# Performance work log

Measured on AMD Instinct MI355X. Metric: run time of the kernel, lower is better.

The kernel has to match this reference:

```python
import jax, jax.numpy as jnp
import numpy as np

NUM_HEADS = 16
NUM_GROUPS = 32  # min(C//4, 32) with C=1024
EPS = 1e-6       # flax GroupNorm default


def setup_inputs() -> dict:
    key = jax.random.key(0)
    ks = jax.random.split(key, 3)
    B, L, C = 2, 2048, 1024
    x = jax.random.normal(ks[0], (B, L, C), dtype=jnp.float32)
    gn_scale = jnp.ones((C,), jnp.float32)
    gn_bias = jnp.zeros((C,), jnp.float32)
    qkv_w = jax.random.normal(ks[1], (C, 3 * C), jnp.float32) * (C ** -0.5)
    qkv_b = jnp.zeros((3 * C,), jnp.float32)
    proj_w = jax.random.normal(ks[2], (C, C), jnp.float32) * 1e-5  # default_init(1e-10) ~ tiny
    proj_b = jnp.zeros((C,), jnp.float32)
    return {"x": x, "gn_scale": gn_scale, "gn_bias": gn_bias,
            "qkv_w": qkv_w, "qkv_b": qkv_b, "proj_w": proj_w, "proj_b": proj_b}


def reference(x, gn_scale, gn_bias, qkv_w, qkv_b, proj_w, proj_b):
    B, L, C = x.shape
    H = NUM_HEADS
    hd = C // H
    # GroupNorm over (L, channels-in-group)
    xg = x.reshape(B, L, NUM_GROUPS, C // NUM_GROUPS)
    mu = jnp.mean(xg, axis=(1, 3), keepdims=True)
    var = jnp.var(xg, axis=(1, 3), keepdims=True)
    xn = ((xg - mu) * jax.lax.rsqrt(var + EPS)).reshape(B, L, C)
    xn = xn * gn_scale + gn_bias
    # 1x1-conv QKV projection == dense
    qkv = xn @ qkv_w + qkv_b                       # [B, L, 3C]
    qkv = qkv.reshape(B, L, H, 3 * hd)             # interleaved per-head q|k|v
    q, k, v = jnp.split(qkv, 3, axis=-1)           # each [B, L, H, hd]
    scale = 1.0 / jnp.sqrt(hd)
    logits = jnp.einsum('btnh,bfnh->bnft', k, q * scale)  # [B, H, L, L]
    weights = jax.nn.softmax(logits, axis=-1)
    h = jnp.einsum('bnft,btnh->bfnh', weights, v).reshape(B, L, C)
    h = h @ proj_w + proj_b
    # CombineResidualSkip, project_skip=False
    return (x + h) / np.sqrt(2.0)
```

## Files before the change

### kernel.cpp

```cpp
#include <hip/hip_runtime.h>
#include <hip/hip_bf16.h>

typedef __hip_bfloat16 bf16;
typedef __attribute__((ext_vector_type(8))) __bf16 bf16x8;
typedef __attribute__((ext_vector_type(4))) float floatx4;

#define NB 2
#define NL 2048
#define NC 1024
#define NH 16
#define ND 64

__device__ __forceinline__ void async_copy16(void* lds, const void* g) {
  __builtin_amdgcn_global_load_lds(
      (__attribute__((address_space(1))) void*)(const_cast<void*>(g)),
      (__attribute__((address_space(3))) void*)(lds), 16, 0, 0);
}

__device__ __forceinline__ floatx4 mfma16(bf16x8 a, bf16x8 b, floatx4 c) {
  return __builtin_amdgcn_mfma_f32_16x16x32_bf16(a, b, c, 0, 0, 0);
}

__global__ __launch_bounds__(256) void gn_part_kernel(
    const float* __restrict__ x, float2* __restrict__ part) {
  int bg = blockIdx.x >> 3, sl = blockIdx.x & 7;
  int b = bg >> 5, g = bg & 31;
  const float* base = x + (size_t)b * NL * NC + (size_t)(sl * 256) * NC + g * 32;
  float s = 0.f, ss = 0.f;
  for (int vi = threadIdx.x; vi < 2048; vi += 256) {
    int l = vi >> 3, j = (vi & 7) * 4;
    float4 u = *(const float4*)(base + (size_t)l * NC + j);
    s += u.x + u.y + u.z + u.w;
    ss += u.x * u.x + u.y * u.y + u.z * u.z + u.w * u.w;
  }
  for (int off = 32; off; off >>= 1) {
    s += __shfl_down(s, off);
    ss += __shfl_down(ss, off);
  }
  __shared__ float rs[4], rss[4];
  int wave = threadIdx.x >> 6, lane = threadIdx.x & 63;
  if (lane == 0) { rs[wave] = s; rss[wave] = ss; }
  __syncthreads();
  if (threadIdx.x == 0) {
    part[blockIdx.x] = make_float2(rs[0] + rs[1] + rs[2] + rs[3],
                                   rss[0] + rss[1] + rss[2] + rss[3]);
  }
}

__global__ __launch_bounds__(256) void gn_apply_kernel(
    const float* __restrict__ x, const float2* __restrict__ part,
    const float* __restrict__ scale, const float* __restrict__ bias,
    bf16* __restrict__ xn) {
  size_t idx = (size_t)blockIdx.x * 256 + threadIdx.x;
  size_t e = idx * 8;
  int c = (int)(e & (NC - 1));
  int b = (int)(e >> 21);
  int bg = b * 32 + (c >> 5);
  float s = 0.f, ss = 0.f;
#pragma unroll
  for (int i = 0; i < 8; ++i) {
    float2 p = part[bg * 8 + i];
    s += p.x; ss += p.y;
  }
  float mean = s * (1.f / 65536.f);
  float var = ss * (1.f / 65536.f) - mean * mean;
  float rstd = rsqrtf(var + 1e-6f);
  float4 x0 = *(const float4*)(x + e);
  float4 x1 = *(const float4*)(x + e + 4);
  float4 s0 = *(const float4*)(scale + c);
  float4 s1 = *(const float4*)(scale + c + 4);
  float4 b0 = *(const float4*)(bias + c);
  float4 b1 = *(const float4*)(bias + c + 4);
  float xv[8] = {x0.x, x0.y, x0.z, x0.w, x1.x, x1.y, x1.z, x1.w};
  float sv[8] = {s0.x, s0.y, s0.z, s0.w, s1.x, s1.y, s1.z, s1.w};
  float bv[8] = {b0.x, b0.y, b0.z, b0.w, b1.x, b1.y, b1.z, b1.w};
  bf16 o[8];
#pragma unroll
  for (int k = 0; k < 8; ++k)
    o[k] = __float2bfloat16((xv[k] - mean) * rstd * sv[k] + bv[k]);
  *(uint4*)(xn + e) = *(const uint4*)o;
}

__global__ void transpose_f32_bf16(const float* __restrict__ in,
                                   bf16* __restrict__ out, int R, int C) {
  __shared__ float t[32][33];
  int c0 = blockIdx.x * 32, r0 = blockIdx.y * 32;
#pragma unroll
  for (int j = 0; j < 4; ++j)
    t[threadIdx.y + j * 8][threadIdx.x] =
        in[(size_t)(r0 + threadIdx.y + j * 8) * C + c0 + threadIdx.x];
  __syncthreads();
#pragma unroll
  for (int j = 0; j < 4; ++j)
    out[(size_t)(c0 + threadIdx.y + j * 8) * R + r0 + threadIdx.x] =
        __float2bfloat16(t[threadIdx.x][threadIdx.y + j * 8]);
}

template <int MODE, int NT>
__global__ __launch_bounds__(256) void gemm_kernel(
    const bf16* __restrict__ A, const bf16* __restrict__ Bt,
    const float* __restrict__ biasv, const float* __restrict__ xres,
    bf16* __restrict__ Qo, bf16* __restrict__ Ko, bf16* __restrict__ Vto,
    float* __restrict__ out, int M, int N, int K) {
  constexpr int NFR = NT / 32;
  __shared__ bf16 As[128 * 32];
  __shared__ bf16 Bs[NT * 32];
  int tid = threadIdx.x, wave = tid >> 6, lane = tid & 63;
  int col = lane & 15, quad = lane >> 4;
  int mB = blockIdx.y * 128, nB = blockIdx.x * NT;
  int wm = (wave >> 1) * 64, wn = (wave & 1) * (NT / 2);
  floatx4 acc[4][NFR];
#pragma unroll
  for (int i = 0; i < 4; ++i)
#pragma unroll
    for (int j = 0; j < NFR; ++j) acc[i][j] = (floatx4){0.f, 0.f, 0.f, 0.f};

  int rowOff = wave * 32 + (lane >> 2);
  int rowOffB = (NT == 128) ? rowOff : (wave * 16 + (lane >> 2));
  int kOff = (lane & 3) * 8;

  for (int k0 = 0; k0 < K; k0 += 32) {
    __syncthreads();
    const bf16* ga = A + (size_t)(mB + rowOff) * K + k0 + kOff;
    async_copy16(&As[(wave * 32) * 32], ga);
    async_copy16(&As[(wave * 32 + 16) * 32], ga + (size_t)16 * K);
    const bf16* gb = Bt + (size_t)(nB + rowOffB) * K + k0 + kOff;
    if (NT == 128) {
      async_copy16(&Bs[(wave * 32) * 32], gb);
      async_copy16(&Bs[(wave * 32 + 16) * 32], gb + (size_t)16 * K);
    } else {
      async_copy16(&Bs[(wave * 16) * 32], gb);
    }
    __syncthreads();
    bf16x8 af[4], bfr[NFR];
#pragma unroll
    for (int mi = 0; mi < 4; ++mi)
      af[mi] = *(const bf16x8*)&As[(wm + mi * 16 + col) * 32 + quad * 8];
#pragma unroll
    for (int ni = 0; ni < NFR; ++ni)
      bfr[ni] = *(const bf16x8*)&Bs[(wn + ni * 16 + col) * 32 + quad * 8];
#pragma unroll
    for (int mi = 0; mi < 4; ++mi)
#pragma unroll
      for (int ni = 0; ni < NFR; ++ni)
        acc[mi][ni] = mfma16(af[mi], bfr[ni], acc[mi][ni]);
  }

#pragma unroll
  for (int mi = 0; mi < 4; ++mi)
#pragma unroll
    for (int ni = 0; ni < NFR; ++ni)
#pragma unroll
      for (int r = 0; r < 4; ++r) {
        int row = mB + wm + mi * 16 + quad * 4 + r;
        int ncol = nB + wn + ni * 16 + col;
        float v = acc[mi][ni][r] + biasv[ncol];
        if (MODE == 0) {
          int b = row >> 11, f = row & 2047;
          int h = ncol / 192, rr = ncol - h * 192;
          size_t bhl = ((size_t)(b * NH + h) * NL + f);
          if (rr < 64)
            Qo[bhl * 64 + rr] = __float2bfloat16(v * 0.125f);
          else if (rr < 128)
            Ko[bhl * 64 + rr - 64] = __float2bfloat16(v);
          else
            Vto[((size_t)(b * NH + h) * 64 + (rr - 128)) * NL + f] = __float2bfloat16(v);
        } else {
          size_t o = (size_t)row * N + ncol;
          out[o] = (xres[o] + v) * 0.70710678118654752f;
        }
      }
}

__global__ __launch_bounds__(512, 2) void attn_kernel(
    const bf16* __restrict__ Q, const bf16* __restrict__ Kb,
    const bf16* __restrict__ Vt, bf16* __restrict__ hout) {
  int qt = blockIdx.x, bh = blockIdx.y;
  int b = bh >> 4, h = bh & 15;
  int tid = threadIdx.x, wave = tid >> 6, lane = tid & 63;
  int m = lane & 15, quad = lane >> 4;

  __shared__ bf16 Kd[2][4096];
  __shared__ bf16 Vd[2][4096];
  __shared__ bf16 Pp[8][2048];

  bf16* Psw = Pp[wave];

  const bf16* Kg = Kb + (size_t)bh * NL * 64;
  const bf16* Vg = Vt + (size_t)bh * 64 * NL;

  bf16x8 bq[2][2];
  {
    const bf16* Qg = Q + ((size_t)bh * NL + qt * 256 + wave * 32) * 64;
#pragma unroll
    for (int nf = 0; nf < 2; ++nf)
#pragma unroll
      for (int c = 0; c < 2; ++c)
        bq[nf][c] = *(const bf16x8*)&Qg[(size_t)(nf * 16 + m) * 64 + c * 32 + quad * 8];
  }

  float lrow[2] = {0.f, 0.f};
  floatx4 o[2][4];
#pragma unroll
  for (int nf = 0; nf < 2; ++nf)
#pragma unroll
    for (int di = 0; di < 4; ++di) o[nf][di] = (floatx4){0.f, 0.f, 0.f, 0.f};

  int srow = lane >> 3, schunk = lane & 7;

  auto stage = [&](int bufi, int t0) {
    int r0 = wave * 8;
    int r = r0 + srow;
    int cg = schunk ^ (r & 7);
    async_copy16(&Kd[bufi][r0 * 64], Kg + (size_t)(t0 + r) * 64 + cg * 8);
    async_copy16(&Vd[bufi][r0 * 64], Vg + (size_t)r * NL + t0 + cg * 8);
  };

  stage(0, 0);
  __syncthreads();

  int buf = 0;
  for (int t0 = 0; t0 < NL; t0 += 64) {
    if (t0 + 64 < NL) stage(buf ^ 1, t0 + 64);

    const bf16* Kbase = Kd[buf];
    const bf16* Vbase = Vd[buf];

    floatx4 s[2][4];
#pragma unroll
    for (int nf = 0; nf < 2; ++nf)
#pragma unroll
      for (int ti = 0; ti < 4; ++ti) s[nf][ti] = (floatx4){0.f, 0.f, 0.f, 0.f};
#pragma unroll
    for (int ti = 0; ti < 4; ++ti)
#pragma unroll
      for (int c = 0; c < 2; ++c) {
        bf16x8 ak = *(const bf16x8*)
            &Kbase[(ti * 16 + m) * 64 + ((c * 4 + quad) ^ (m & 7)) * 8];
        s[0][ti] = mfma16(ak, bq[0][c], s[0][ti]);
        s[1][ti] = mfma16(ak, bq[1][c], s[1][ti]);
      }

#pragma unroll
    for (int nf = 0; nf < 2; ++nf) {
      float ls = 0.f;
#pragma unroll
      for (int ti = 0; ti < 4; ++ti)
#pragma unroll
        for (int r = 0; r < 4; ++r) {
          float p = __expf(s[nf][ti][r]);
          s[nf][ti][r] = p;
          ls += p;
        }
      ls += __shfl_xor(ls, 16);
      ls += __shfl_xor(ls, 32);
      lrow[nf] += ls;
#pragma unroll
      for (int ti = 0; ti < 4; ++ti) {
        bf16 pk[4];
#pragma unroll
        for (int r = 0; r < 4; ++r) pk[r] = __float2bfloat16(s[nf][ti][r]);
        int ct = ti * 2 + (quad >> 1);
        *(uint2*)&Psw[(nf * 16 + m) * 64 + ((ct ^ (m & 7)) * 8) + (quad & 1) * 4] =
            *(const uint2*)pk;
      }
    }

#pragma unroll
    for (int c = 0; c < 2; ++c) {
      bf16x8 bp[2];
#pragma unroll
      for (int nf = 0; nf < 2; ++nf)
        bp[nf] = *(const bf16x8*)
            &Psw[(nf * 16 + m) * 64 + (((c * 4 + quad) ^ (m & 7)) * 8)];
#pragma unroll
      for (int di = 0; di < 4; ++di) {
        bf16x8 av = *(const bf16x8*)
            &Vbase[(di * 16 + m) * 64 + ((c * 4 + quad) ^ (m & 7)) * 8];
        o[0][di] = mfma16(av, bp[0], o[0][di]);
        o[1][di] = mfma16(av, bp[1], o[1][di]);
      }
    }

    __syncthreads();
    buf ^= 1;
  }

#pragma unroll
  for (int nf = 0; nf < 2; ++nf) {
    float rl = 1.f / lrow[nf];
    int l = qt * 256 + wave * 32 + nf * 16 + m;
    bf16* hp = hout + (size_t)(b * NL + l) * NC + h * 64;
#pragma unroll
    for (int di = 0; di < 4; ++di) {
      bf16 pk[4];
#pragma unroll
      for (int r = 0; r < 4; ++r) pk[r] = __float2bfloat16(o[nf][di][r] * rl);
      *(uint2*)&hp[di * 16 + quad * 4] = *(const uint2*)pk;
    }
  }
}

extern "C" void kernel_launch(void* const* d_in, const int* in_sizes, int n_in,
                              void* d_out, int out_size, void* d_ws, size_t ws_size,
                              hipStream_t stream) {
  const float* x = (const float*)d_in[0];
  const float* gn_scale = (const float*)d_in[1];
  const float* gn_bias = (const float*)d_in[2];
  const float* qkv_w = (const float*)d_in[3];
  const float* qkv_b = (const float*)d_in[4];
  const float* proj_w = (const float*)d_in[5];
  const float* proj_b = (const float*)d_in[6];
  float* out = (float*)d_out;

  bf16* xn = (bf16*)d_out;

  char* ws = (char*)d_ws;
  float2* part = (float2*)ws;
  bf16* Qb = (bf16*)(ws + 4096);
  bf16* Kbuf = Qb + 4194304;
  bf16* Vt = Kbuf + 4194304;
  bf16* hat = Vt + 4194304;
  bf16* wqkvT = hat;
  bf16* projT = Qb;

  gn_part_kernel<<<512, 256, 0, stream>>>(x, part);
  gn_apply_kernel<<<2048, 256, 0, stream>>>(x, part, gn_scale, gn_bias, xn);
  transpose_f32_bf16<<<dim3(96, 32), dim3(32, 8), 0, stream>>>(qkv_w, wqkvT, 1024, 3072);
  gemm_kernel<0, 128><<<dim3(24, 32), 256, 0, stream>>>(
      xn, wqkvT, qkv_b, nullptr, Qb, Kbuf, Vt, nullptr, 4096, 3072, 1024);
  attn_kernel<<<dim3(8, 32), 512, 0, stream>>>(Qb, Kbuf, Vt, hat);
  transpose_f32_bf16<<<dim3(32, 32), dim3(32, 8), 0, stream>>>(proj_w, projT, 1024, 1024);
  gemm_kernel<1, 64><<<dim3(16, 32), 256, 0, stream>>>(
      hat, projT, proj_b, x, nullptr, nullptr, nullptr, out, 4096, 1024, 1024);
}
```

Before: 218.2 us.

## Process 128 keys per attention iteration, use exp2 with folded log2e scale, vectorize V store

The attention loop now stages and processes 128 keys per iteration as two 64-key halves. This doubles the K/V/P shared buffers and halves the number of block barriers, and launch bounds are relaxed to one block per CU. Q is pre-scaled by log2(e)/8 in the QKV epilogue so the softmax can use exp2f instead of __expf. The V-transpose store is packed into one 8-byte write per fragment. The trade-off is larger shared memory and register use, which lowers occupancy.

```diff
diff --git a/kernel.cpp b/kernel.cpp
--- a/kernel.cpp
+++ b/kernel.cpp
@@ -149,30 +149,42 @@
 #pragma unroll
   for (int mi = 0; mi < 4; ++mi)
 #pragma unroll
-    for (int ni = 0; ni < NFR; ++ni)
-#pragma unroll
-      for (int r = 0; r < 4; ++r) {
-        int row = mB + wm + mi * 16 + quad * 4 + r;
-        int ncol = nB + wn + ni * 16 + col;
-        float v = acc[mi][ni][r] + biasv[ncol];
-        if (MODE == 0) {
-          int b = row >> 11, f = row & 2047;
-          int h = ncol / 192, rr = ncol - h * 192;
-          size_t bhl = ((size_t)(b * NH + h) * NL + f);
-          if (rr < 64)
-            Qo[bhl * 64 + rr] = __float2bfloat16(v * 0.125f);
-          else if (rr < 128)
-            Ko[bhl * 64 + rr - 64] = __float2bfloat16(v);
-          else
-            Vto[((size_t)(b * NH + h) * 64 + (rr - 128)) * NL + f] = __float2bfloat16(v);
+    for (int ni = 0; ni < NFR; ++ni) {
+      int row0 = mB + wm + mi * 16 + quad * 4;
+      int ncol = nB + wn + ni * 16 + col;
+      float vv[4];
+#pragma unroll
+      for (int r = 0; r < 4; ++r) vv[r] = acc[mi][ni][r] + biasv[ncol];
+      if (MODE == 0) {
+        int b = row0 >> 11, f0 = row0 & 2047;
+        int h = ncol / 192, rr = ncol - h * 192;
+        size_t bh = (size_t)(b * NH + h);
+        if (rr < 64) {
+#pragma unroll
+          for (int r = 0; r < 4; ++r)
+            Qo[(bh * NL + f0 + r) * 64 + rr] =
+                __float2bfloat16(vv[r] * 0.18033688011112042f);
+        } else if (rr < 128) {
+#pragma unroll
+          for (int r = 0; r < 4; ++r)
+            Ko[(bh * NL + f0 + r) * 64 + rr - 64] = __float2bfloat16(vv[r]);
         } else {
-          size_t o = (size_t)row * N + ncol;
-          out[o] = (xres[o] + v) * 0.70710678118654752f;
+          bf16 pk[4];
+#pragma unroll
+          for (int r = 0; r < 4; ++r) pk[r] = __float2bfloat16(vv[r]);
+          *(uint2*)&Vto[(bh * 64 + (rr - 128)) * NL + f0] = *(const uint2*)pk;
         }
-      }
-}
-
-__global__ __launch_bounds__(512, 2) void attn_kernel(
+      } else {
+#pragma unroll
+        for (int r = 0; r < 4; ++r) {
+          size_t o = (size_t)(row0 + r) * N + ncol;
+          out[o] = (xres[o] + vv[r]) * 0.70710678118654752f;
+        }
+      }
+    }
+}
+
+__global__ __launch_bounds__(512, 1) void attn_kernel(
     const bf16* __restrict__ Q, const bf16* __restrict__ Kb,
     const bf16* __restrict__ Vt, bf16* __restrict__ hout) {
   int qt = blockIdx.x, bh = blockIdx.y;
@@ -180,11 +192,12 @@
   int tid = threadIdx.x, wave = tid >> 6, lane = tid & 63;
   int m = lane & 15, quad = lane >> 4;
 
-  __shared__ bf16 Kd[2][4096];
-  __shared__ bf16 Vd[2][4096];
-  __shared__ bf16 Pp[8][2048];
-
-  bf16* Psw = Pp[wave];
+  __shared__ bf16 Kd[2][8192];
+  __shared__ bf16 Vd[2][8192];
+  __shared__ bf16 Pp[8][4096];
+
+  bf16* Pa = Pp[wave];
+  bf16* Pb = Pp[wave] + 2048;
 
   const bf16* Kg = Kb + (size_t)bh * NL * 64;
   const bf16* Vg = Vt + (size_t)bh * 64 * NL;
@@ -209,36 +222,49 @@
   int srow = lane >> 3, schunk = lane & 7;
 
   auto stage = [&](int bufi, int t0) {
-    int r0 = wave * 8;
-    int r = r0 + srow;
-    int cg = schunk ^ (r & 7);
-    async_copy16(&Kd[bufi][r0 * 64], Kg + (size_t)(t0 + r) * 64 + cg * 8);
-    async_copy16(&Vd[bufi][r0 * 64], Vg + (size_t)r * NL + t0 + cg * 8);
+#pragma unroll
+    for (int i = 0; i < 2; ++i) {
+      int r0 = wave * 16 + i * 8;
+      int r = r0 + srow;
+      int cg = schunk ^ (r & 7);
+      async_copy16(&Kd[bufi][r0 * 64], Kg + (size_t)(t0 + r) * 64 + cg * 8);
+      int sub = r >> 6, d = r & 63;
+      async_copy16(&Vd[bufi][r0 * 64], Vg + (size_t)d * NL + t0 + sub * 64 + cg * 8);
+    }
   };
 
   stage(0, 0);
   __syncthreads();
 
   int buf = 0;
-  for (int t0 = 0; t0 < NL; t0 += 64) {
-    if (t0 + 64 < NL) stage(buf ^ 1, t0 + 64);
-
-    const bf16* Kbase = Kd[buf];
-    const bf16* Vbase = Vd[buf];
-
-    floatx4 s[2][4];
+  for (int t0 = 0; t0 < NL; t0 += 128) {
+    if (t0 + 128 < NL) stage(buf ^ 1, t0 + 128);
+
+    const bf16* Ka = &Kd[buf][0];
+    const bf16* Kb2 = &Kd[buf][4096];
+    const bf16* Va = &Vd[buf][0];
+    const bf16* Vb2 = &Vd[buf][4096];
+
+    floatx4 sa[2][4], sb[2][4];
 #pragma unroll
     for (int nf = 0; nf < 2; ++nf)
 #pragma unroll
-      for (int ti = 0; ti < 4; ++ti) s[nf][ti] = (floatx4){0.f, 0.f, 0.f, 0.f};
+      for (int ti = 0; ti < 4; ++ti) {
+        sa[nf][ti] = (floatx4){0.f, 0.f, 0.f, 0.f};
+        sb[nf][ti] = (floatx4){0.f, 0.f, 0.f, 0.f};
+      }
 #pragma unroll
     for (int ti = 0; ti < 4; ++ti)
 #pragma unroll
       for (int c = 0; c < 2; ++c) {
         bf16x8 ak = *(const bf16x8*)
-            &Kbase[(ti * 16 + m) * 64 + ((c * 4 + quad) ^ (m & 7)) * 8];
-        s[0][ti] = mfma16(ak, bq[0][c], s[0][ti]);
-        s[1][ti] = mfma16(ak, bq[1][c], s[1][ti]);
+            &Ka[(ti * 16 + m) * 64 + ((c * 4 + quad) ^ (m & 7)) * 8];
+        sa[0][ti] = mfma16(ak, bq[0][c], sa[0][ti]);
+        sa[1][ti] = mfma16(ak, bq[1][c], sa[1][ti]);
+        bf16x8 ak2 = *(const bf16x8*)
+            &Kb2[(ti * 16 + m) * 64 + ((c * 4 + quad) ^ (m & 7)) * 8];
+        sb[0][ti] = mfma16(ak2, bq[0][c], sb[0][ti]);
+        sb[1][ti] = mfma16(ak2, bq[1][c], sb[1][ti]);
       }
 
 #pragma unroll
@@ -248,8 +274,8 @@
       for (int ti = 0; ti < 4; ++ti)
 #pragma unroll
         for (int r = 0; r < 4; ++r) {
-          float p = __expf(s[nf][ti][r]);
-          s[nf][ti][r] = p;
+          float p = exp2f(sa[nf][ti][r]);
+          sa[nf][ti][r] = p;
           ls += p;
         }
       ls += __shfl_xor(ls, 16);
@@ -259,9 +285,33 @@
       for (int ti = 0; ti < 4; ++ti) {
         bf16 pk[4];
 #pragma unroll
-        for (int r = 0; r < 4; ++r) pk[r] = __float2bfloat16(s[nf][ti][r]);
+        for (int r = 0; r < 4; ++r) pk[r] = __float2bfloat16(sa[nf][ti][r]);
         int ct = ti * 2 + (quad >> 1);
-        *(uint2*)&Psw[(nf * 16 + m) * 64 + ((ct ^ (m & 7)) * 8) + (quad & 1) * 4] =
+        *(uint2*)&Pa[(nf * 16 + m) * 64 + ((ct ^ (m & 7)) * 8) + (quad & 1) * 4] =
+            *(const uint2*)pk;
+      }
+    }
+#pragma unroll
+    for (int nf = 0; nf < 2; ++nf) {
+      float ls = 0.f;
+#pragma unroll
+      for (int ti = 0; ti < 4; ++ti)
+#pragma unroll
+        for (int r = 0; r < 4; ++r) {
+          float p = exp2f(sb[nf][ti][r]);
+          sb[nf][ti][r] = p;
+          ls += p;
+        }
+      ls += __shfl_xor(ls, 16);
+      ls += __shfl_xor(ls, 32);
+      lrow[nf] += ls;
+#pragma unroll
+      for (int ti = 0; ti < 4; ++ti) {
+        bf16 pk[4];
+#pragma unroll
+        for (int r = 0; r < 4; ++r) pk[r] = __float2bfloat16(sb[nf][ti][r]);
+        int ct = ti * 2 + (quad >> 1);
+        *(uint2*)&Pb[(nf * 16 + m) * 64 + ((ct ^ (m & 7)) * 8) + (quad & 1) * 4] =
             *(const uint2*)pk;
       }
     }
@@ -272,11 +322,26 @@
 #pragma unroll
       for (int nf = 0; nf < 2; ++nf)
         bp[nf] = *(const bf16x8*)
-            &Psw[(nf * 16 + m) * 64 + (((c * 4 + quad) ^ (m & 7)) * 8)];
+            &Pa[(nf * 16 + m) * 64 + (((c * 4 + quad) ^ (m & 7)) * 8)];
 #pragma unroll
       for (int di = 0; di < 4; ++di) {
         bf16x8 av = *(const bf16x8*)
-            &Vbase[(di * 16 + m) * 64 + ((c * 4 + quad) ^ (m & 7)) * 8];
+            &Va[(di * 16 + m) * 64 + ((c * 4 + quad) ^ (m & 7)) * 8];
+        o[0][di] = mfma16(av, bp[0], o[0][di]);
+        o[1][di] = mfma16(av, bp[1], o[1][di]);
+      }
+    }
+#pragma unroll
+    for (int c = 0; c < 2; ++c) {
+      bf16x8 bp[2];
+#pragma unroll
+      for (int nf = 0; nf < 2; ++nf)
+        bp[nf] = *(const bf16x8*)
+            &Pb[(nf * 16 + m) * 64 + (((c * 4 + quad) ^ (m & 7)) * 8)];
+#pragma unroll
+      for (int di = 0; di < 4; ++di) {
+        bf16x8 av = *(const bf16x8*)
+            &Vb2[(di * 16 + m) * 64 + ((c * 4 + quad) ^ (m & 7)) * 8];
         o[0][di] = mfma16(av, bp[0], o[0][di]);
         o[1][di] = mfma16(av, bp[1], o[1][di]);
       }
```

New measurement: 223.2 us. 1.02x slower.
